# Kernel optimization log

Measured on AMD Instinct MI355X. Metric: run time of the kernel, lower is better.

Reference implementation:

```python
import jax, jax.numpy as jnp
import numpy as np

NUM_HEADS = 16
EPS = 1e-6


def setup_inputs() -> dict:
    key = jax.random.key(0)
    ks = jax.random.split(key, 5)
    L, N, E = 2048, 8, 1024
    scale = 1.0 / np.sqrt(E)
    return {
        "query": jax.random.normal(ks[0], (L, N, E), jnp.float32),
        "Wq": jax.random.normal(ks[1], (E, E), jnp.float32) * scale,
        "Wk": jax.random.normal(ks[2], (E, E), jnp.float32) * scale,
        "Wv": jax.random.normal(ks[3], (E, E), jnp.float32) * scale,
        "Wo": jax.random.normal(ks[4], (E, E), jnp.float32) * scale,
    }


def reference(query, Wq, Wk, Wv, Wo):
    # cosFormer non-causal linear attention (self.causal = False branch).
    L, N, E = query.shape
    h = NUM_HEADS
    d = E // h

    # projections (nn.Linear, no bias) + ReLU feature map on q, k
    q = jax.nn.relu(query @ Wq.T)
    k = jax.nn.relu(query @ Wk.T)  # key defaults to query
    v = query @ Wv.T               # value defaults to query

    # (L, N, E) -> (n = N*h, L, d)
    def split_heads(x):
        return x.reshape(L, N * h, d).transpose(1, 0, 2)

    q, k, v = split_heads(q), split_heads(k), split_heads(v)

    # cos/sin reweighting: index = pi/2 * arange(1..m) / m, m = L (src==tgt)
    idx = (jnp.pi / 2) * jnp.arange(1, L + 1, dtype=jnp.float32) / L
    sin = jnp.sin(idx)[None, :, None]  # (1, L, 1)
    cos = jnp.cos(idx)[None, :, None]
    q_ = jnp.concatenate([q * sin, q * cos], axis=-1)  # (n, L, 2d)
    k_ = jnp.concatenate([k * sin, k * cos], axis=-1)

    # linear attention aggregation: kv_ is only (n, 2d, d)
    kv = jnp.einsum('nld,nlm->ndm', k_, v)
    z = 1.0 / jnp.maximum(jnp.einsum('nld,nd->nl', q_, k_.sum(axis=1)), EPS)
    attn = jnp.einsum('nld,ndm->nlm', q_, kv) * z[..., None]  # (n, L, d)

    # (n, L, d) -> (L, N, E), then output projection
    attn = attn.transpose(1, 0, 2).reshape(L, N, E)
    return attn @ Wo.T
```

## Files before the change

kernel.cpp:

```cpp
#include <hip/hip_runtime.h>
#include <math.h>

#define L_DIM 2048
#define N_DIM 8
#define E_DIM 1024
#define H_DIM 16
#define D_DIM 64
#define M_DIM (L_DIM * N_DIM)
#define NHEADS (N_DIM * H_DIM)
#define TWO_D 128
#define K_DIM 1024
#define CH 4
#define LCH (L_DIM / CH)

#define KV_ELEMS (NHEADS * TWO_D * D_DIM)
#define KS_ELEMS (NHEADS * TWO_D)
#define CSTRIDE (KV_ELEMS + KS_ELEMS)

typedef __attribute__((ext_vector_type(8))) __bf16 bf16x8;
typedef __attribute__((ext_vector_type(4))) float f32x4;
typedef __attribute__((ext_vector_type(8))) ushort u16x8;

__device__ __forceinline__ ushort f2bf(float x) {
    union { float f; unsigned u; } a; a.f = x;
    unsigned r = a.u + 0x7fffu + ((a.u >> 16) & 1u);
    return (ushort)(r >> 16);
}
__device__ __forceinline__ float bf2f(ushort h) {
    union { unsigned u; float f; } a; a.u = ((unsigned)h) << 16;
    return a.f;
}

__device__ __forceinline__ void gload_lds16(const void* g, void* l) {
    __builtin_amdgcn_global_load_lds((const __attribute__((address_space(1))) void*)g,
                                     (__attribute__((address_space(3))) void*)l, 16, 0, 0);
}

__global__ __launch_bounds__(256) void split_all(const float* __restrict__ X,
                                                 const float* __restrict__ W0,
                                                 const float* __restrict__ W1,
                                                 const float* __restrict__ W2,
                                                 const float* __restrict__ W3,
                                                 ushort* __restrict__ Xhi,
                                                 ushort* __restrict__ Xlo,
                                                 ushort* __restrict__ Whi,
                                                 ushort* __restrict__ Wlo) {
    const int NX4 = M_DIM * E_DIM / 4;
    const int NW4 = E_DIM * E_DIM / 4;
    const int total = NX4 + 4 * NW4;
    int i = blockIdx.x * 256 + threadIdx.x;
    const int stride = gridDim.x * 256;
    for (; i < total; i += stride) {
        const float4* src;
        ushort4 *dhi, *dlo;
        int idx;
        if (i < NX4) {
            src = (const float4*)X;
            dhi = (ushort4*)Xhi;
            dlo = (ushort4*)Xlo;
            idx = i;
        } else {
            const int r = i - NX4;
            const int w = r >> 18;
            idx = r & (NW4 - 1);
            const float* ws_ = (w == 0) ? W0 : (w == 1) ? W1 : (w == 2) ? W2 : W3;
            src = (const float4*)ws_;
            dhi = (ushort4*)(Whi + (size_t)w * E_DIM * E_DIM);
            dlo = (ushort4*)(Wlo + (size_t)w * E_DIM * E_DIM);
        }
        float4 v = src[idx];
        ushort h0 = f2bf(v.x), h1 = f2bf(v.y), h2 = f2bf(v.z), h3 = f2bf(v.w);
        ushort l0 = f2bf(v.x - bf2f(h0)), l1 = f2bf(v.y - bf2f(h1));
        ushort l2 = f2bf(v.z - bf2f(h2)), l3 = f2bf(v.w - bf2f(h3));
        dhi[idx] = make_ushort4(h0, h1, h2, h3);
        dlo[idx] = make_ushort4(l0, l1, l2, l3);
    }
}

template <int OUTMODE, int NBS>
__global__ __launch_bounds__(512, 2) void gemm2(const ushort* __restrict__ Ahi,
                                                const ushort* __restrict__ Alo,
                                                const ushort* __restrict__ Bhi,
                                                const ushort* __restrict__ Blo,
                                                float* __restrict__ C,
                                                float* __restrict__ C2) {
    __shared__ ushort smem[2][32768];

    const int t = threadIdx.x;
    const int wid = t >> 6;
    const int lane = t & 63;

    const int x = blockIdx.x;
    const int cxcd = x & 7;
    const int j = x >> 3;
    const int mb = cxcd * 8 + j / NBS;
    const int nb = j % NBS;
    const int m0 = mb * 256, n0 = nb * 256;

    const int srow = t >> 2;
    const int sch = t & 3;
    const int gch = sch ^ ((srow >> 1) & 3);
    const size_t aOff = (size_t)(m0 + srow) * K_DIM + gch * 8;
    const size_t bOff = (size_t)(n0 + srow) * K_DIM + gch * 8;
    const size_t H128 = (size_t)128 * K_DIM;

#define STAGE(b, kt1)                                             \
    do {                                                          \
        const size_t kc_ = (size_t)(kt1) * 32;                    \
        ushort* d = (ushort*)&smem[b][0] + wid * 512;             \
        gload_lds16(Ahi + aOff + kc_, d);                         \
        gload_lds16(Ahi + aOff + H128 + kc_, d + 4096);           \
        gload_lds16(Alo + aOff + kc_, d + 8192);                  \
        gload_lds16(Alo + aOff + H128 + kc_, d + 12288);          \
        gload_lds16(Bhi + bOff + kc_, d + 16384);                 \
        gload_lds16(Bhi + bOff + H128 + kc_, d + 20480);          \
        gload_lds16(Blo + bOff + kc_, d + 24576);                 \
        gload_lds16(Blo + bOff + H128 + kc_, d + 28672);          \
    } while (0)

    const int wm = wid >> 2;
    const int wn = wid & 3;
    const int lr = lane & 15;
    const int kc = lane >> 4;
    int aoff[8], boff[4];
#pragma unroll
    for (int m = 0; m < 8; ++m) {
        const int r = wm * 128 + m * 16 + lr;
        aoff[m] = r * 32 + ((kc ^ ((r >> 1) & 3)) << 3);
    }
#pragma unroll
    for (int n = 0; n < 4; ++n) {
        const int r = wn * 64 + n * 16 + lr;
        boff[n] = r * 32 + ((kc ^ ((r >> 1) & 3)) << 3);
    }

    f32x4 acc[8][4];
    const f32x4 zv = {0.f, 0.f, 0.f, 0.f};
#pragma unroll
    for (int m = 0; m < 8; ++m)
#pragma unroll
        for (int n = 0; n < 4; ++n) acc[m][n] = zv;

    const int NK = K_DIM / 32;

    STAGE(0, 0);
    __syncthreads();

#pragma unroll 1
    for (int kt = 0; kt < NK; ++kt) {
        const int cb = kt & 1;
        if (kt + 1 < NK) STAGE(cb ^ 1, kt + 1);

        const ushort* bb = smem[cb];
        bf16x8 bh[4], bl[4];
#pragma unroll
        for (int n = 0; n < 4; ++n) {
            bh[n] = *(const bf16x8*)&bb[16384 + boff[n]];
            bl[n] = *(const bf16x8*)&bb[24576 + boff[n]];
        }
#pragma unroll
        for (int m = 0; m < 8; ++m) {
            const bf16x8 ah = *(const bf16x8*)&bb[aoff[m]];
            const bf16x8 al = *(const bf16x8*)&bb[8192 + aoff[m]];
#pragma unroll
            for (int n = 0; n < 4; ++n) {
                acc[m][n] = __builtin_amdgcn_mfma_f32_16x16x32_bf16(ah, bh[n], acc[m][n], 0, 0, 0);
                acc[m][n] = __builtin_amdgcn_mfma_f32_16x16x32_bf16(ah, bl[n], acc[m][n], 0, 0, 0);
                acc[m][n] = __builtin_amdgcn_mfma_f32_16x16x32_bf16(al, bh[n], acc[m][n], 0, 0, 0);
            }
        }
        __syncthreads();
    }

    const int erow = (lane >> 4) * 4;
    const int ecol = lane & 15;
#pragma unroll
    for (int m = 0; m < 8; ++m) {
        const int grb = m0 + wm * 128 + m * 16 + erow;
#pragma unroll
        for (int n = 0; n < 4; ++n) {
            const int gc = n0 + wn * 64 + n * 16 + ecol;
            f32x4 v = acc[m][n];
#pragma unroll
            for (int q = 0; q < 4; ++q) {
                const int gr = grb + q;
                float val = v[q];
                if constexpr (OUTMODE == 0) {
                    C[(size_t)gr * E_DIM + gc] = val;
                } else if constexpr (OUTMODE == 1) {
                    val = fmaxf(val, 0.f);
                    const int hh = gc >> 6, d = gc & 63;
                    C[((size_t)((gr & 7) * 16 + hh) * L_DIM + (gr >> 3)) * D_DIM + d] = val;
                } else {
                    const int mat = gc >> 10;
                    const int col = gc & 1023;
                    if (mat == 0) val = fmaxf(val, 0.f);
                    const int hh = col >> 6, d = col & 63;
                    float* dstc = mat ? C2 : C;
                    dstc[((size_t)((gr & 7) * 16 + hh) * L_DIM + (gr >> 3)) * D_DIM + d] = val;
                }
            }
        }
    }
#undef STAGE
}

__global__ __launch_bounds__(256) void kv_partial(const float* __restrict__ Kh,
                                                  const float* __restrict__ Vh,
                                                  float* __restrict__ kvp) {
    const int g = blockIdx.x;
    const int c = blockIdx.y;
    const int t = threadIdx.x;

    __shared__ float Kt[2][32][64];
    __shared__ float Vt[2][32][64];
    __shared__ float sT[2][32], cT[2][32];

    const int gi = t >> 3;
    const int gj = t & 7;
    const int i0 = gi * 2, j0 = gj * 8;

    float S[2][8], Cc[2][8];
#pragma unroll
    for (int i = 0; i < 2; ++i)
#pragma unroll
        for (int jj = 0; jj < 8; ++jj) { S[i][jj] = 0.f; Cc[i][jj] = 0.f; }
    float sk[2] = {0.f, 0.f}, ck[2] = {0.f, 0.f};

    const int NIT = LCH / 32;
    float4 rk0, rk1, rv0, rv1;
    float rs = 0.f, rc_ = 0.f;

#define LOADT(it)                                                              \
    do {                                                                       \
        const int lbase_ = c * LCH + (it) * 32;                                \
        const float4* ks_ = (const float4*)&Kh[((size_t)g * L_DIM + lbase_) * D_DIM]; \
        const float4* vs_ = (const float4*)&Vh[((size_t)g * L_DIM + lbase_) * D_DIM]; \
        rk0 = ks_[t]; rk1 = ks_[t + 256];                                      \
        rv0 = vs_[t]; rv1 = vs_[t + 256];                                      \
        if (t < 32) {                                                          \
            const float ang_ = 1.57079632679489662f * (float)(lbase_ + t + 1) / (float)L_DIM; \
            rs = sinf(ang_); rc_ = cosf(ang_);                                 \
        }                                                                      \
    } while (0)

    LOADT(0);
#pragma unroll 1
    for (int it = 0; it < NIT; ++it) {
        const int b = it & 1;
        ((float4*)&Kt[b][0][0])[t] = rk0;
        ((float4*)&Kt[b][0][0])[t + 256] = rk1;
        ((float4*)&Vt[b][0][0])[t] = rv0;
        ((float4*)&Vt[b][0][0])[t + 256] = rv1;
        if (t < 32) { sT[b][t] = rs; cT[b][t] = rc_; }
        if (it + 1 < NIT) LOADT(it + 1);
        __syncthreads();

#pragma unroll 4
        for (int lr = 0; lr < 32; ++lr) {
            const float sl = sT[b][lr], cl = cT[b][lr];
            const float k0v = Kt[b][lr][i0], k1v = Kt[b][lr][i0 + 1];
            const float ks0 = k0v * sl, ks1 = k1v * sl;
            const float kc0 = k0v * cl, kc1 = k1v * cl;
            sk[0] += ks0; sk[1] += ks1; ck[0] += kc0; ck[1] += kc1;
            float v8[8];
            *(float4*)&v8[0] = *(float4*)&Vt[b][lr][j0];
            *(float4*)&v8[4] = *(float4*)&Vt[b][lr][j0 + 4];
#pragma unroll
            for (int jj = 0; jj < 8; ++jj) {
                S[0][jj] = fmaf(ks0, v8[jj], S[0][jj]);
                S[1][jj] = fmaf(ks1, v8[jj], S[1][jj]);
                Cc[0][jj] = fmaf(kc0, v8[jj], Cc[0][jj]);
                Cc[1][jj] = fmaf(kc1, v8[jj], Cc[1][jj]);
            }
        }
    }
#undef LOADT

    float* kvb = kvp + (size_t)c * CSTRIDE + (size_t)g * TWO_D * D_DIM;
#pragma unroll
    for (int ii = 0; ii < 2; ++ii) {
        *(float4*)&kvb[(size_t)(i0 + ii) * D_DIM + j0] =
            make_float4(S[ii][0], S[ii][1], S[ii][2], S[ii][3]);
        *(float4*)&kvb[(size_t)(i0 + ii) * D_DIM + j0 + 4] =
            make_float4(S[ii][4], S[ii][5], S[ii][6], S[ii][7]);
        *(float4*)&kvb[(size_t)(64 + i0 + ii) * D_DIM + j0] =
            make_float4(Cc[ii][0], Cc[ii][1], Cc[ii][2], Cc[ii][3]);
        *(float4*)&kvb[(size_t)(64 + i0 + ii) * D_DIM + j0 + 4] =
            make_float4(Cc[ii][4], Cc[ii][5], Cc[ii][6], Cc[ii][7]);
    }
    if (gj == 0) {
        float* ksb = kvp + (size_t)c * CSTRIDE + KV_ELEMS + (size_t)g * TWO_D;
        ksb[i0] = sk[0];
        ksb[i0 + 1] = sk[1];
        ksb[64 + i0] = ck[0];
        ksb[64 + i0 + 1] = ck[1];
    }
}

__global__ __launch_bounds__(256) void attn_mfma(const float* __restrict__ Qh,
                                                 const float* __restrict__ kvp,
                                                 ushort* __restrict__ attnHi,
                                                 ushort* __restrict__ attnLo) {
    const int g = blockIdx.x;
    const int ltg = blockIdx.y;
    const int nb = g >> 4, hh = g & 15;
    const int t = threadIdx.x;
    const int wid = t >> 6, lane = t & 63;

    __shared__ ushort kvbH[4][64][32];
    __shared__ ushort kvbL[4][64][32];
    __shared__ ushort qaH[4][64][32];
    __shared__ ushort qaL[4][64][32];
    __shared__ float ksS[TWO_D];
    __shared__ float pz[64][4];
    __shared__ float zs[64];

    if (t < TWO_D) {
        const size_t o = KV_ELEMS + (size_t)g * TWO_D + t;
        ksS[t] = kvp[o] + kvp[o + CSTRIDE] + kvp[o + 2 * (size_t)CSTRIDE] +
                 kvp[o + 3 * (size_t)CSTRIDE];
    }

    {
        const float* kvg = kvp + (size_t)g * TWO_D * D_DIM;
        const int d = t & 63;
        const int igb = t >> 6;
        const int csd = (d >> 1) & 3;
#pragma unroll
        for (int rep = 0; rep < 4; ++rep) {
            const int i0 = (rep * 4 + igb) * 8;
            float v[8];
#pragma unroll
            for (int jj = 0; jj < 8; ++jj) {
                const size_t o = (size_t)(i0 + jj) * D_DIM + d;
                v[jj] = kvg[o] + kvg[o + CSTRIDE] + kvg[o + 2 * (size_t)CSTRIDE] +
                        kvg[o + 3 * (size_t)CSTRIDE];
            }
            const int ks = i0 >> 5;
            const int cs = ((((i0 >> 3) & 3) ^ csd) << 3);
            u16x8 h, l;
#pragma unroll
            for (int jj = 0; jj < 8; ++jj) {
                h[jj] = f2bf(v[jj]);
                l[jj] = f2bf(v[jj] - bf2f(h[jj]));
            }
            *(u16x8*)&kvbH[ks][d][cs] = h;
            *(u16x8*)&kvbL[ks][d][cs] = l;
        }
    }

    const int lq = t >> 2;
    const int dq = (t & 3) * 16;
    const int csq = (lq >> 1) & 3;

    const int lr = lane & 15, kc = lane >> 4;
    const int arow = wid * 16 + lr;
    const int aco = ((kc ^ ((arow >> 1) & 3)) << 3);
    int bro[4], bco[4];
#pragma unroll
    for (int n = 0; n < 4; ++n) {
        bro[n] = n * 16 + lr;
        bco[n] = ((kc ^ ((bro[n] >> 1) & 3)) << 3);
    }
    const int erow = (lane >> 4) * 4;
    const int ecol = lane & 15;

    __syncthreads();

#pragma unroll 1
    for (int it = 0; it < 4; ++it) {
        const int lbase = (ltg * 4 + it) * 64;

        float qv[16];
        const float* qrow = Qh + ((size_t)g * L_DIM + lbase + lq) * D_DIM + dq;
        *(float4*)&qv[0] = *(const float4*)&qrow[0];
        *(float4*)&qv[4] = *(const float4*)&qrow[4];
        *(float4*)&qv[8] = *(const float4*)&qrow[8];
        *(float4*)&qv[12] = *(const float4*)&qrow[12];
        const float ang = 1.57079632679489662f * (float)(lbase + lq + 1) / (float)L_DIM;
        const float sl = sinf(ang), cl = cosf(ang);

        float p = 0.f;
#pragma unroll
        for (int jj = 0; jj < 16; ++jj)
            p += qv[jj] * (sl * ksS[dq + jj] + cl * ksS[64 + dq + jj]);
        pz[lq][t & 3] = p;

#pragma unroll
        for (int jg = 0; jg < 2; ++jg) {
            const int ib = dq + jg * 8;
            const int ks = ib >> 5;
            const int cs = ((((ib >> 3) & 3) ^ csq) << 3);
            u16x8 hs, ls, hc, lc;
#pragma unroll
            for (int jj = 0; jj < 8; ++jj) {
                const float vs = qv[jg * 8 + jj] * sl;
                const float vc = qv[jg * 8 + jj] * cl;
                hs[jj] = f2bf(vs); ls[jj] = f2bf(vs - bf2f(hs[jj]));
                hc[jj] = f2bf(vc); lc[jj] = f2bf(vc - bf2f(hc[jj]));
            }
            *(u16x8*)&qaH[ks][lq][cs] = hs;
            *(u16x8*)&qaL[ks][lq][cs] = ls;
            *(u16x8*)&qaH[ks + 2][lq][cs] = hc;
            *(u16x8*)&qaL[ks + 2][lq][cs] = lc;
        }
        __syncthreads();
        if (t < 64) {
            const float s = pz[t][0] + pz[t][1] + pz[t][2] + pz[t][3];
            zs[t] = 1.0f / fmaxf(s, 1e-6f);
        }
        __syncthreads();

        f32x4 acc[4];
        const f32x4 zv = {0.f, 0.f, 0.f, 0.f};
#pragma unroll
        for (int n = 0; n < 4; ++n) acc[n] = zv;
#pragma unroll
        for (int ks = 0; ks < 4; ++ks) {
            const bf16x8 ah = *(const bf16x8*)&qaH[ks][arow][aco];
            const bf16x8 al = *(const bf16x8*)&qaL[ks][arow][aco];
#pragma unroll
            for (int n = 0; n < 4; ++n) {
                const bf16x8 bh = *(const bf16x8*)&kvbH[ks][bro[n]][bco[n]];
                const bf16x8 bl = *(const bf16x8*)&kvbL[ks][bro[n]][bco[n]];
                acc[n] = __builtin_amdgcn_mfma_f32_16x16x32_bf16(ah, bh, acc[n], 0, 0, 0);
                acc[n] = __builtin_amdgcn_mfma_f32_16x16x32_bf16(ah, bl, acc[n], 0, 0, 0);
                acc[n] = __builtin_amdgcn_mfma_f32_16x16x32_bf16(al, bh, acc[n], 0, 0, 0);
            }
        }

#pragma unroll
        for (int n = 0; n < 4; ++n) {
#pragma unroll
            for (int q = 0; q < 4; ++q) {
                const int lrow = wid * 16 + erow + q;
                const float val = acc[n][q] * zs[lrow];
                const int d = n * 16 + ecol;
                const ushort hv = f2bf(val);
                const ushort lv = f2bf(val - bf2f(hv));
                const size_t base = (size_t)((lbase + lrow) * N_DIM + nb) * E_DIM + hh * 64 + d;
                attnHi[base] = hv;
                attnLo[base] = lv;
            }
        }
        __syncthreads();
    }
}

extern "C" void kernel_launch(void* const* d_in, const int* in_sizes, int n_in,
                              void* d_out, int out_size, void* d_ws, size_t ws_size,
                              hipStream_t stream) {
    const float* X = (const float*)d_in[0];
    const float* Wq = (const float*)d_in[1];
    const float* Wk = (const float*)d_in[2];
    const float* Wv = (const float*)d_in[3];
    const float* Wo = (const float*)d_in[4];
    float* out = (float*)d_out;

    char* ws = (char*)d_ws;
    ushort* Xhi = (ushort*)(ws + 0);
    ushort* Xlo = (ushort*)(ws + 33554432);
    ushort* Whi = (ushort*)(ws + 67108864);
    ushort* Wlo = (ushort*)(ws + 75497472);
    float* kvp  = (float*)(ws + 83886080);
    float* bufA = (float*)(ws + 100925440);

    float* Kh = out;
    float* Vh = bufA;
    float* Qh = out;

    const size_t WMAT = (size_t)E_DIM * E_DIM;

    split_all<<<2048, 256, 0, stream>>>(X, Wq, Wk, Wv, Wo, Xhi, Xlo, Whi, Wlo);

    gemm2<2, 8><<<512, 512, 0, stream>>>(Xhi, Xlo, Whi + 1 * WMAT, Wlo + 1 * WMAT, Kh, Vh);

    kv_partial<<<dim3(NHEADS, CH), 256, 0, stream>>>(Kh, Vh, kvp);

    gemm2<1, 4><<<256, 512, 0, stream>>>(Xhi, Xlo, Whi + 0 * WMAT, Wlo + 0 * WMAT, Qh, nullptr);

    attn_mfma<<<dim3(NHEADS, L_DIM / 256), 256, 0, stream>>>(Qh, kvp, Xhi, Xlo);

    gemm2<0, 4><<<256, 512, 0, stream>>>(Xhi, Xlo, Whi + 3 * WMAT, Wlo + 3 * WMAT, out, nullptr);
}
```

Before: 464.4 us.

## Deepen GEMM prefetch pipeline with triple-buffered A tiles and explicit vmcnt waits

Splits the shared LDS staging buffer into separate A and B buffers, with A triple-buffered and B double-buffered. Loads are issued two K-steps ahead for A and one for B. The full __syncthreads is replaced by targeted s_waitcnt vmcnt counts plus s_barrier, so later loads can stay in flight across the barrier. The aim is to hide more global-memory latency behind the MFMA work. The cost is LDS growing from 128 KB to 160 KB per block, and synchronisation that depends on hand-counted outstanding loads.

```diff
diff --git a/kernel.cpp b/kernel.cpp
--- a/kernel.cpp
+++ b/kernel.cpp
@@ -84,7 +84,8 @@
                                                 const ushort* __restrict__ Blo,
                                                 float* __restrict__ C,
                                                 float* __restrict__ C2) {
-    __shared__ ushort smem[2][32768];
+    __shared__ ushort As[3][16384];
+    __shared__ ushort Bs[2][16384];
 
     const int t = threadIdx.x;
     const int wid = t >> 6;
@@ -104,18 +105,24 @@
     const size_t bOff = (size_t)(n0 + srow) * K_DIM + gch * 8;
     const size_t H128 = (size_t)128 * K_DIM;
 
-#define STAGE(b, kt1)                                             \
+#define STAGE_A(bi, kt1)                                          \
     do {                                                          \
         const size_t kc_ = (size_t)(kt1) * 32;                    \
-        ushort* d = (ushort*)&smem[b][0] + wid * 512;             \
+        ushort* d = &As[bi][0] + wid * 512;                       \
         gload_lds16(Ahi + aOff + kc_, d);                         \
         gload_lds16(Ahi + aOff + H128 + kc_, d + 4096);           \
         gload_lds16(Alo + aOff + kc_, d + 8192);                  \
         gload_lds16(Alo + aOff + H128 + kc_, d + 12288);          \
-        gload_lds16(Bhi + bOff + kc_, d + 16384);                 \
-        gload_lds16(Bhi + bOff + H128 + kc_, d + 20480);          \
-        gload_lds16(Blo + bOff + kc_, d + 24576);                 \
-        gload_lds16(Blo + bOff + H128 + kc_, d + 28672);          \
+    } while (0)
+
+#define STAGE_B(bi, kt1)                                          \
+    do {                                                          \
+        const size_t kc_ = (size_t)(kt1) * 32;                    \
+        ushort* d = &Bs[bi][0] + wid * 512;                       \
+        gload_lds16(Bhi + bOff + kc_, d);                         \
+        gload_lds16(Bhi + bOff + H128 + kc_, d + 4096);           \
+        gload_lds16(Blo + bOff + kc_, d + 8192);                  \
+        gload_lds16(Blo + bOff + H128 + kc_, d + 12288);          \
     } while (0)
 
     const int wm = wid >> 2;
@@ -143,25 +150,31 @@
 
     const int NK = K_DIM / 32;
 
-    STAGE(0, 0);
-    __syncthreads();
+    STAGE_B(0, 0);
+    STAGE_A(0, 0);
+    STAGE_B(1, 1);
+    STAGE_A(1, 1);
+    asm volatile("s_waitcnt vmcnt(8)" ::: "memory");
+    __builtin_amdgcn_s_barrier();
+    asm volatile("" ::: "memory");
 
 #pragma unroll 1
     for (int kt = 0; kt < NK; ++kt) {
-        const int cb = kt & 1;
-        if (kt + 1 < NK) STAGE(cb ^ 1, kt + 1);
-
-        const ushort* bb = smem[cb];
+        if (kt >= 1 && kt + 1 < NK) STAGE_B((kt + 1) & 1, kt + 1);
+        if (kt + 2 < NK) STAGE_A((kt + 2) % 3, kt + 2);
+
+        const ushort* ab = &As[kt % 3][0];
+        const ushort* bbuf = &Bs[kt & 1][0];
         bf16x8 bh[4], bl[4];
 #pragma unroll
         for (int n = 0; n < 4; ++n) {
-            bh[n] = *(const bf16x8*)&bb[16384 + boff[n]];
-            bl[n] = *(const bf16x8*)&bb[24576 + boff[n]];
+            bh[n] = *(const bf16x8*)&bbuf[boff[n]];
+            bl[n] = *(const bf16x8*)&bbuf[8192 + boff[n]];
         }
 #pragma unroll
         for (int m = 0; m < 8; ++m) {
-            const bf16x8 ah = *(const bf16x8*)&bb[aoff[m]];
-            const bf16x8 al = *(const bf16x8*)&bb[8192 + aoff[m]];
+            const bf16x8 ah = *(const bf16x8*)&ab[aoff[m]];
+            const bf16x8 al = *(const bf16x8*)&ab[8192 + aoff[m]];
 #pragma unroll
             for (int n = 0; n < 4; ++n) {
                 acc[m][n] = __builtin_amdgcn_mfma_f32_16x16x32_bf16(ah, bh[n], acc[m][n], 0, 0, 0);
@@ -169,7 +182,16 @@
                 acc[m][n] = __builtin_amdgcn_mfma_f32_16x16x32_bf16(al, bh[n], acc[m][n], 0, 0, 0);
             }
         }
-        __syncthreads();
+
+        if (kt < NK - 1) {
+            if (kt + 2 < NK) {
+                asm volatile("s_waitcnt vmcnt(4)" ::: "memory");
+            } else {
+                asm volatile("s_waitcnt vmcnt(0)" ::: "memory");
+            }
+            __builtin_amdgcn_s_barrier();
+            asm volatile("" ::: "memory");
+        }
     }
 
     const int erow = (lane >> 4) * 4;
@@ -202,7 +224,8 @@
             }
         }
     }
-#undef STAGE
+#undef STAGE_A
+#undef STAGE_B
 }
 
 __global__ __launch_bounds__(256) void kv_partial(const float* __restrict__ Kh,
```

Measured after the change: 512.9 us. 10.4% more time.
